# Optimization experiments

Hardware: AMD Instinct MI355X
Metric: run time of the kernel (lower is better)

Reference implementation:

```python
import jax, jax.numpy as jnp
import numpy as np
from jax import lax

AR_ORDER = 8
SEQ_LEN = 4096
BATCH = 8192
REGRESSOR_DIM = AR_ORDER + 1  # ar_order past outputs + 1 (zeroed) exogenous term


def setup_inputs() -> dict:
    key = jax.random.key(0)
    k1, k2, k3 = jax.random.split(key, 3)
    y = jax.random.normal(k1, (BATCH, AR_ORDER), dtype=jnp.float32)
    u = jax.random.normal(k2, (BATCH, SEQ_LEN), dtype=jnp.float32)
    # scale weights so the linear recurrence is stable over 4096 steps
    W = jax.random.normal(k3, (1, REGRESSOR_DIM), dtype=jnp.float32) * 0.05
    return {"y": y, "u": u, "W": W}


def reference(y, u, W):
    # Faithful ARX forward: output[:, :ar] = y, then for each t,
    ar = y.shape[1]
    seq = u.shape[1]
    w_ar = W[0, :ar]          # coefficients on past outputs
    # W[0, ar] multiplies the zeroed exogenous term -> contributes 0

    def step(carry, _):
        # carry: [B, ar] = last ar outputs (oldest first)
        pred = carry @ w_ar                                   # [B]
        new_carry = jnp.concatenate([carry[:, 1:], pred[:, None]], axis=1)
        return new_carry, pred

    _, preds = lax.scan(step, y, xs=None, length=seq)         # preds: [seq, B]
    return jnp.concatenate([y, preds.T], axis=1)              # [B, seq + ar]
```

## Files before the change

kernel.cpp:

```cpp
#include <hip/hip_runtime.h>

#define AR 8
#define SEQ 4096
#define BATCH 8192
#define OUTW (AR + SEQ)

typedef float f32x4 __attribute__((ext_vector_type(4)));

__global__ __launch_bounds__(256) void coeff_kernel(const float* __restrict__ W,
                                                    float* __restrict__ C) {
    __shared__ float P[12][AR][AR];
    __shared__ float w[AR];
    const int tid = threadIdx.x;

    if (tid < AR) w[tid] = W[tid];
    __syncthreads();

    if (tid < 64) {
        const int i = tid >> 3, j = tid & 7;
        P[0][i][j] = (i == 7) ? w[j] : ((i == j - 1) ? 1.f : 0.f);
    }
    __syncthreads();

    for (int k = 0; k < 11; ++k) {
        if (tid < 64) {
            const int i = tid >> 3, j = tid & 7;
            float v = 0.f;
            #pragma unroll
            for (int q = 0; q < AR; ++q) v += P[k][i][q] * P[k][q][j];
            P[k + 1][i][j] = v;
        }
        __syncthreads();
    }

    const int t = blockIdx.x * 256 + tid;
    float r[AR];
    #pragma unroll
    for (int j = 0; j < AR; ++j) r[j] = w[j];
    #pragma unroll
    for (int k = 0; k < 12; ++k) {
        if ((t >> k) & 1) {
            float nr[AR];
            #pragma unroll
            for (int j = 0; j < AR; ++j) {
                float s = 0.f;
                #pragma unroll
                for (int q = 0; q < AR; ++q) s += r[q] * P[k][q][j];
                nr[j] = s;
            }
            #pragma unroll
            for (int j = 0; j < AR; ++j) r[j] = nr[j];
        }
    }

    f32x4* dst = reinterpret_cast<f32x4*>(C);
    dst[(size_t)t * 2 + 0] = (f32x4){r[0], r[1], r[2], r[3]};
    dst[(size_t)t * 2 + 1] = (f32x4){r[4], r[5], r[6], r[7]};
}

__global__ __launch_bounds__(256) void pred_kernel(const float* __restrict__ y,
                                                   const float* __restrict__ C,
                                                   float* __restrict__ out) {
    const int tt = blockIdx.x * 256 + threadIdx.x;
    const int t0 = tt * 4;

    float c[4][AR];
    const f32x4* Cv = reinterpret_cast<const f32x4*>(C + (size_t)t0 * AR);
    #pragma unroll
    for (int k = 0; k < 4; ++k) {
        f32x4 a = Cv[k * 2 + 0];
        f32x4 b = Cv[k * 2 + 1];
        c[k][0] = a.x; c[k][1] = a.y; c[k][2] = a.z; c[k][3] = a.w;
        c[k][4] = b.x; c[k][5] = b.y; c[k][6] = b.z; c[k][7] = b.w;
    }

    for (int rg = blockIdx.y; rg < BATCH / 8; rg += gridDim.y) {
        const int row0 = rg * 8;

        float yy[8][AR];
        #pragma unroll
        for (int r = 0; r < 8; ++r) {
            const f32x4* yv = reinterpret_cast<const f32x4*>(y + (size_t)(row0 + r) * AR);
            f32x4 a = yv[0], b = yv[1];
            yy[r][0] = a.x; yy[r][1] = a.y; yy[r][2] = a.z; yy[r][3] = a.w;
            yy[r][4] = b.x; yy[r][5] = b.y; yy[r][6] = b.z; yy[r][7] = b.w;
        }

        #pragma unroll
        for (int r = 0; r < 8; ++r) {
            float s[4];
            #pragma unroll
            for (int k = 0; k < 4; ++k) {
                float acc = 0.f;
                #pragma unroll
                for (int j = 0; j < AR; ++j) acc += c[k][j] * yy[r][j];
                s[k] = acc;
            }
            *reinterpret_cast<f32x4*>(out + (size_t)(row0 + r) * OUTW + AR + t0) =
                (f32x4){s[0], s[1], s[2], s[3]};
        }

        if (blockIdx.x == 0 && threadIdx.x < 16) {
            const int r = threadIdx.x >> 1, part = threadIdx.x & 1;
            const int row = row0 + r;
            reinterpret_cast<f32x4*>(out + (size_t)row * OUTW)[part] =
                reinterpret_cast<const f32x4*>(y + (size_t)row * AR)[part];
        }
    }
}

extern "C" void kernel_launch(void* const* d_in, const int* in_sizes, int n_in,
                              void* d_out, int out_size, void* d_ws, size_t ws_size,
                              hipStream_t stream) {
    const float* y = (const float*)d_in[0];
    const float* W = (const float*)d_in[2];
    float* out = (float*)d_out;
    float* C = (float*)d_ws;

    coeff_kernel<<<SEQ / 256, 256, 0, stream>>>(W, C);
    pred_kernel<<<dim3(SEQ / 1024, 256), 256, 0, stream>>>(y, C, out);
}
```

Before: 31.78 us.

## Fuse coefficient generation into prediction kernel and derive neighbors by companion shift

Merges the coefficient kernel into the prediction kernel, so each block rebuilds the 12 companion-matrix powers in shared memory and computes its own coefficient rows. The workspace write/read and the second launch go away. Each thread runs the binary-power product only for its base timestep and gets the next three by a cheap one-step companion update. In exchange every one of the 1024 blocks repeats the 11 serial 8x8 matrix squarings with syncs, which adds startup latency per block.

```diff
diff --git a/kernel.cpp b/kernel.cpp
--- a/kernel.cpp
+++ b/kernel.cpp
@@ -7,8 +7,9 @@
 
 typedef float f32x4 __attribute__((ext_vector_type(4)));
 
-__global__ __launch_bounds__(256) void coeff_kernel(const float* __restrict__ W,
-                                                    float* __restrict__ C) {
+__global__ __launch_bounds__(256, 4) void arx_fused_kernel(const float* __restrict__ y,
+                                                           const float* __restrict__ W,
+                                                           float* __restrict__ out) {
     __shared__ float P[12][AR][AR];
     __shared__ float w[AR];
     const int tid = threadIdx.x;
@@ -33,45 +34,38 @@
         __syncthreads();
     }
 
-    const int t = blockIdx.x * 256 + tid;
-    float r[AR];
-    #pragma unroll
-    for (int j = 0; j < AR; ++j) r[j] = w[j];
-    #pragma unroll
-    for (int k = 0; k < 12; ++k) {
-        if ((t >> k) & 1) {
-            float nr[AR];
-            #pragma unroll
-            for (int j = 0; j < AR; ++j) {
-                float s = 0.f;
-                #pragma unroll
-                for (int q = 0; q < AR; ++q) s += r[q] * P[k][q][j];
-                nr[j] = s;
-            }
-            #pragma unroll
-            for (int j = 0; j < AR; ++j) r[j] = nr[j];
-        }
-    }
-
-    f32x4* dst = reinterpret_cast<f32x4*>(C);
-    dst[(size_t)t * 2 + 0] = (f32x4){r[0], r[1], r[2], r[3]};
-    dst[(size_t)t * 2 + 1] = (f32x4){r[4], r[5], r[6], r[7]};
-}
-
-__global__ __launch_bounds__(256) void pred_kernel(const float* __restrict__ y,
-                                                   const float* __restrict__ C,
-                                                   float* __restrict__ out) {
-    const int tt = blockIdx.x * 256 + threadIdx.x;
+    const int tt = blockIdx.x * 256 + tid;
     const int t0 = tt * 4;
 
     float c[4][AR];
-    const f32x4* Cv = reinterpret_cast<const f32x4*>(C + (size_t)t0 * AR);
-    #pragma unroll
-    for (int k = 0; k < 4; ++k) {
-        f32x4 a = Cv[k * 2 + 0];
-        f32x4 b = Cv[k * 2 + 1];
-        c[k][0] = a.x; c[k][1] = a.y; c[k][2] = a.z; c[k][3] = a.w;
-        c[k][4] = b.x; c[k][5] = b.y; c[k][6] = b.z; c[k][7] = b.w;
+    {
+        float r[AR];
+        #pragma unroll
+        for (int j = 0; j < AR; ++j) r[j] = w[j];
+        #pragma unroll
+        for (int k = 2; k < 12; ++k) {
+            if ((t0 >> k) & 1) {
+                float nr[AR];
+                #pragma unroll
+                for (int j = 0; j < AR; ++j) {
+                    float s = 0.f;
+                    #pragma unroll
+                    for (int q = 0; q < AR; ++q) s += r[q] * P[k][q][j];
+                    nr[j] = s;
+                }
+                #pragma unroll
+                for (int j = 0; j < AR; ++j) r[j] = nr[j];
+            }
+        }
+        #pragma unroll
+        for (int j = 0; j < AR; ++j) c[0][j] = r[j];
+        #pragma unroll
+        for (int k = 1; k < 4; ++k) {
+            const float c7 = c[k - 1][AR - 1];
+            c[k][0] = c7 * w[0];
+            #pragma unroll
+            for (int j = 1; j < AR; ++j) c[k][j] = c[k - 1][j - 1] + c7 * w[j];
+        }
     }
 
     for (int rg = blockIdx.y; rg < BATCH / 8; rg += gridDim.y) {
@@ -115,8 +109,6 @@
     const float* y = (const float*)d_in[0];
     const float* W = (const float*)d_in[2];
     float* out = (float*)d_out;
-    float* C = (float*)d_ws;
 
-    coeff_kernel<<<SEQ / 256, 256, 0, stream>>>(W, C);
-    pred_kernel<<<dim3(SEQ / 1024, 256), 256, 0, stream>>>(y, C, out);
+    arx_fused_kernel<<<dim3(SEQ / 1024, 256), 256, 0, stream>>>(y, W, out);
 }
```

Measured after the change: 27.44 us, median of 2. -13.7%, faster.
